# Optimization experiments

Measured on AMD Instinct MI355X. Metric: run time of the kernel, lower is better.

The kernel has to match this reference:

```python
import jax, jax.numpy as jnp
import numpy as np

N = 100_000        # nodes
E = 1_600_000      # edges
IN_F = 128         # input_features
HID = 64           # hiddens per head
OUT = 64           # outputs
NHEADS = 8
ALPHA = 0.2        # leaky_relu negative slope


def setup_inputs() -> dict:
    key = jax.random.key(0)
    ks = jax.random.split(key, 8)
    x = jax.random.normal(ks[0], (N, IN_F), jnp.float32)
    edges = jax.random.randint(ks[1], (2, E), 0, N)
    # nn.Linear(input_features, input_features)
    W0 = jax.random.normal(ks[2], (IN_F, IN_F), jnp.float32) / np.sqrt(IN_F).astype(np.float32)
    b0 = jnp.zeros((IN_F,), jnp.float32)
    # per-head SpGAT params: W [in, out], a [2*out]
    W_heads = jax.random.normal(ks[3], (NHEADS, IN_F, HID), jnp.float32) * 0.05
    a_heads = jax.random.normal(ks[4], (NHEADS, 2 * HID), jnp.float32) * 0.05
    W_end = jax.random.normal(ks[5], (NHEADS * HID, OUT), jnp.float32) * 0.05
    a_end = jax.random.normal(ks[6], (2 * OUT,), jnp.float32) * 0.05
    return dict(x=x, edges=edges, W0=W0, b0=b0,
                W_heads=W_heads, a_heads=a_heads, W_end=W_end, a_end=a_end)


def _sp_gat_layer(x, src, dst, W, a, apply_elu):
    """Standard sparse GAT layer (pyGAT SpGraphAttentionLayer).

    score_e = a . [h_src || h_dst];  e = exp(-leaky_relu(score))
    out_i = (sum_{e: src=i} e * h_dst) / (sum_{e: src=i} e)
    """
    n = x.shape[0]
    h = x @ W                      # [N, F]
    F = h.shape[1]
    # a.[h_i||h_j] decomposed into per-node scores to avoid [E, 2F] gather
    s_src = h @ a[:F]              # [N]
    s_dst = h @ a[F:]              # [N]
    score = s_src[src] + s_dst[dst]            # [E]
    edge_e = jnp.exp(-jax.nn.leaky_relu(score, ALPHA))
    rowsum = jax.ops.segment_sum(edge_e, src, num_segments=n)            # [N]
    agg = jax.ops.segment_sum(edge_e[:, None] * h[dst], src, num_segments=n)  # [N, F]
    out = agg / (rowsum[:, None] + 1e-16)
    return jax.nn.elu(out) if apply_elu else out


def reference(x, edges, W0, b0, W_heads, a_heads, W_end, a_end):
    src, dst = edges[0], edges[1]
    xp = x @ W0 + b0                                           # self.layer
    # multi-head attention, concat on feature dim (loop over fixed small head count)
    heads = [_sp_gat_layer(xp, src, dst, W_heads[i], a_heads[i], apply_elu=True)
             for i in range(NHEADS)]
    h = jnp.concatenate(heads, axis=1)                         # [N, NHEADS*HID]
    out = _sp_gat_layer(h, src, dst, W_end, a_end, apply_elu=False)  # [N, OUT]
    return jax.nn.softmax(out, axis=1)
```

## Files before the change

kernel.cpp:

```cpp
#include <hip/hip_runtime.h>


using bf16x8 = __bf16 __attribute__((ext_vector_type(8)));
using f32x4  = float  __attribute__((ext_vector_type(4)));

__device__ __forceinline__ unsigned short f2bf(float f) {
    __bf16 h = (__bf16)f;
    return __builtin_bit_cast(unsigned short, h);
}
__device__ __forceinline__ float bflo(unsigned int u) {
    return __builtin_bit_cast(float, u << 16);
}
__device__ __forceinline__ float bfhi(unsigned int u) {
    return __builtin_bit_cast(float, u & 0xffff0000u);
}
__device__ __forceinline__ float bfs(unsigned short u) {
    return __builtin_bit_cast(float, (unsigned)u << 16);
}
__device__ __forceinline__ int rdlane_i(int v, int l) {
    return __builtin_amdgcn_readlane(v, l);
}
__device__ __forceinline__ float rdlane_f(float v, int l) {
    return __builtin_bit_cast(float, __builtin_amdgcn_readlane(__builtin_bit_cast(int, v), l));
}
__device__ __forceinline__ float exp2fast(float x) {
#if __has_builtin(__builtin_amdgcn_exp2f)
    return __builtin_amdgcn_exp2f(x);
#else
    return exp2f(x);
#endif
}

#define ALPHA_NEG 0.2f
#define LOG2E 1.44269504088896340736f
#define CHUNK 20000

__global__ void pack_all(const float* __restrict__ W0, const float* __restrict__ Wh,
                         const float* __restrict__ We, const float* __restrict__ ah,
                         unsigned short* __restrict__ W0t, unsigned short* __restrict__ Ballt,
                         unsigned short* __restrict__ Wendt, unsigned short* __restrict__ Bscore) {
    int b = blockIdx.x, t = threadIdx.x;
    if (b < 64) {
        int idx = b * 256 + t;
        int n = idx >> 7, k = idx & 127;
        W0t[n * 128 + k] = f2bf(W0[k * 128 + n]);
    } else if (b < 320) {
        int idx = (b - 64) * 256 + t;
        int c = idx >> 7, k = idx & 127;
        int h = c >> 6, f = c & 63;
        Ballt[idx] = f2bf(Wh[(h * 128 + k) * 64 + f]);
    } else if (b < 448) {
        int idx = (b - 320) * 256 + t;
        int n = idx >> 9, k = idx & 511;
        Wendt[idx] = f2bf(We[k * 64 + n]);
    } else {
        int idx = (b - 448) * 256 + t;
        if (idx < 1024) {
            int h = idx >> 7, k = idx & 127;
            float s = 0.f, d = 0.f;
            for (int f = 0; f < 64; f++) {
                float wv = Wh[(h * 128 + k) * 64 + f];
                s += wv * ah[h * 128 + f];
                d += wv * ah[h * 128 + 64 + f];
            }
            Bscore[h * 128 + k] = f2bf(s * LOG2E);
            Bscore[(8 + h) * 128 + k] = f2bf(d * LOG2E);
        }
    }
}

__global__ void edge_rank(const int* __restrict__ src, int* __restrict__ deg,
                          int* __restrict__ rank, int E) {
    int i = blockIdx.x * 256 + threadIdx.x;
    if (i >= E) return;
    rank[i] = atomicAdd(&deg[src[i]], 1);
}
__global__ void edge_place(const int* __restrict__ src, const int* __restrict__ dst,
                           const int* __restrict__ row_ptr, const int* __restrict__ rank,
                           int* __restrict__ dstp, int E) {
    int i = blockIdx.x * 256 + threadIdx.x;
    if (i >= E) return;
    dstp[row_ptr[src[i]] + rank[i]] = dst[i];
}

#define SCAN_BS 256
__global__ void scan_blocks(const int* __restrict__ deg, int* __restrict__ incl,
                            int* __restrict__ partials, int n) {
    __shared__ int s[SCAN_BS];
    int t = threadIdx.x, i = blockIdx.x * SCAN_BS + t;
    int v = (i < n) ? deg[i] : 0;
    s[t] = v; __syncthreads();
    for (int off = 1; off < SCAN_BS; off <<= 1) {
        int add = (t >= off) ? s[t - off] : 0;
        __syncthreads();
        s[t] += add;
        __syncthreads();
    }
    if (i < n) incl[i] = s[t];
    if (t == SCAN_BS - 1) partials[blockIdx.x] = s[t];
}
__global__ void scan_partials(int* __restrict__ partials, int nb) {
    __shared__ int s[512];
    int t = threadIdx.x;
    int v = (t < nb) ? partials[t] : 0;
    s[t] = v; __syncthreads();
    for (int off = 1; off < 512; off <<= 1) {
        int add = (t >= off) ? s[t - off] : 0;
        __syncthreads();
        s[t] += add;
        __syncthreads();
    }
    if (t < nb) partials[t] = s[t] - v;
}
__global__ void finalize_rowptr(const int* __restrict__ deg, const int* __restrict__ incl,
                                const int* __restrict__ partials, int* __restrict__ row_ptr,
                                int n, int E) {
    int i = blockIdx.x * 256 + threadIdx.x;
    if (i < n) {
        row_ptr[i] = incl[i] - deg[i] + partials[i / SCAN_BS];
    } else if (i == n) {
        row_ptr[n] = E;
    }
}

template <int BM, int BN, int K, int WM, int WN, int MT, int NT,
          bool AF32, bool BIAS, bool OBF16, bool ELU, bool BATCHZ>
__launch_bounds__(256)
__global__ void gemm_mfma(const void* __restrict__ Ap, const unsigned short* __restrict__ Bt,
                          const float* __restrict__ bias, void* __restrict__ Cp, int M,
                          int lda, int ldc) {
    constexpr int LDK = 40;
    __shared__ unsigned short As[BM * LDK];
    __shared__ unsigned short Bs[BN * LDK];
    const int t = threadIdx.x;
    const long m0 = (long)blockIdx.x * BM;
    const long n0 = (long)blockIdx.y * BN;
    const int abase = BATCHZ ? blockIdx.z * K : 0;
    const unsigned short* Btz = BATCHZ ? Bt + (size_t)blockIdx.z * BN * K : Bt;
    const long cbase = BATCHZ ? (long)blockIdx.z * BN : 0;
    const int wave = t >> 6, lane = t & 63;
    const int wm = wave / WN, wn = wave % WN;
    const int lrow = lane & 15, lq = lane >> 4;

    f32x4 acc[MT][NT];
#pragma unroll
    for (int a = 0; a < MT; a++)
#pragma unroll
        for (int b = 0; b < NT; b++) acc[a][b] = (f32x4)0.0f;

    for (int kt = 0; kt < K / 32; kt++) {
        const int k0 = kt * 32;
        if constexpr (AF32) {
            const float* A = (const float*)Ap;
#pragma unroll
            for (int it = 0; it < BM * 8 / 256; it++) {
                int L = t + 256 * it;
                int row = L >> 3, kc = (L & 7) * 4;
                long gr = m0 + row;
                float4 v = make_float4(0.f, 0.f, 0.f, 0.f);
                if (gr < M) v = *(const float4*)&A[gr * lda + abase + k0 + kc];
                unsigned int lo = (unsigned)f2bf(v.x) | ((unsigned)f2bf(v.y) << 16);
                unsigned int hi = (unsigned)f2bf(v.z) | ((unsigned)f2bf(v.w) << 16);
                *(uint2*)&As[row * LDK + kc] = make_uint2(lo, hi);
            }
        } else {
            const unsigned short* A = (const unsigned short*)Ap;
#pragma unroll
            for (int it = 0; it < BM * 4 / 256; it++) {
                int L = t + 256 * it;
                int row = L >> 2, kc = (L & 3) * 8;
                long gr = m0 + row;
                uint4 v = make_uint4(0u, 0u, 0u, 0u);
                if (gr < M) v = *(const uint4*)&A[gr * lda + abase + k0 + kc];
                *(uint4*)&As[row * LDK + kc] = v;
            }
        }
#pragma unroll
        for (int it = 0; it < (BN * 4 + 255) / 256; it++) {
            int L = t + 256 * it;
            if (L < BN * 4) {
                int row = L >> 2, kc = (L & 3) * 8;
                *(uint4*)&Bs[row * LDK + kc] = *(const uint4*)&Btz[(n0 + row) * K + k0 + kc];
            }
        }
        __syncthreads();

        bf16x8 af[MT], bfr[NT];
#pragma unroll
        for (int mt = 0; mt < MT; mt++)
            af[mt] = *(const bf16x8*)&As[((wm * MT + mt) * 16 + lrow) * LDK + lq * 8];
#pragma unroll
        for (int nt = 0; nt < NT; nt++)
            bfr[nt] = *(const bf16x8*)&Bs[((wn * NT + nt) * 16 + lrow) * LDK + lq * 8];
#pragma unroll
        for (int mt = 0; mt < MT; mt++)
#pragma unroll
            for (int nt = 0; nt < NT; nt++)
                acc[mt][nt] = __builtin_amdgcn_mfma_f32_16x16x32_bf16(af[mt], bfr[nt],
                                                                     acc[mt][nt], 0, 0, 0);
        __syncthreads();
    }

#pragma unroll
    for (int mt = 0; mt < MT; mt++) {
        long rbase = m0 + (wm * MT + mt) * 16 + lq * 4;
#pragma unroll
        for (int nt = 0; nt < NT; nt++) {
            long col = cbase + n0 + (wn * NT + nt) * 16 + lrow;
            float bv = 0.f;
            if constexpr (BIAS) bv = bias[col];
#pragma unroll
            for (int r = 0; r < 4; r++) {
                long row = rbase + r;
                if (row < M) {
                    float v = acc[mt][nt][r] + bv;
                    if constexpr (ELU) v = v > 0.f ? v : __expf(v) - 1.0f;
                    if constexpr (OBF16)
                        ((unsigned short*)Cp)[row * ldc + col] = f2bf(v);
                    else
                        ((float*)Cp)[row * ldc + col] = v;
                }
            }
        }
    }
}

__global__ void agg_xp(const int* __restrict__ row_ptr, const int* __restrict__ dstp,
                       const float* __restrict__ s16,
                       const unsigned short* __restrict__ xp, unsigned short* __restrict__ z,
                       int n0, int n1) {
    int t = threadIdx.x, wave = t >> 6, lane = t & 63;
    int i = n0 + blockIdx.x * 4 + wave;
    if (i >= n1) return;
    int e0 = __builtin_amdgcn_readfirstlane(row_ptr[i]);
    int e1 = __builtin_amdgcn_readfirstlane(row_ptr[i + 1]);
    const int hl = lane & 7, sub8 = lane >> 3;
    const int voff = lane << 1;
    float ssv = s16[(size_t)i * 16 + hl];
    float acc[16];
#pragma unroll
    for (int c = 0; c < 16; c++) acc[c] = 0.f;
    float rsl = 0.f;

    for (int p = e0; p < e1; p += 8) {
        int idx = p + sub8;
        int cl = idx < e1 ? idx : e1 - 1;
        int jv = dstp[cl];
        float sc = s16[(size_t)(unsigned)jv * 16 + 8 + hl];
        float s = ssv + sc;
        s = fmaxf(s, ALPHA_NEG * s);
        float wv = (idx < e1) ? exp2fast(-s) : 0.f;
        rsl += wv;
        int nem = e1 - p;
        unsigned xv[8];
#pragma unroll
        for (int u = 0; u < 8; u++) {
            if (u < nem) {
                int ju = rdlane_i(jv, u * 8);
                xv[u] = *(const unsigned*)&xp[(size_t)(unsigned)ju * 128 + voff];
            }
        }
#pragma unroll
        for (int u = 0; u < 8; u++) {
            if (u < nem) {
                float lo = bflo(xv[u]), hi = bfhi(xv[u]);
#pragma unroll
                for (int h = 0; h < 8; h++) {
                    float wh = rdlane_f(wv, u * 8 + h);
                    acc[2 * h]     += wh * lo;
                    acc[2 * h + 1] += wh * hi;
                }
            }
        }
    }

    rsl += __shfl_xor(rsl, 8, 64);
    rsl += __shfl_xor(rsl, 16, 64);
    rsl += __shfl_xor(rsl, 32, 64);
    float inv = 1.0f / (rsl + 1e-16f);
    size_t zb = (size_t)(i - n0) * 1024 + voff;
#pragma unroll
    for (int h = 0; h < 8; h++) {
        float ih = rdlane_f(inv, h);
        unsigned pw = (unsigned)f2bf(acc[2 * h] * ih) |
                      ((unsigned)f2bf(acc[2 * h + 1] * ih) << 16);
        *(unsigned*)&z[zb + h * 128] = pw;
    }
}

__global__ void scores2(const unsigned short* __restrict__ h2b, const float* __restrict__ ae,
                        float* __restrict__ ss2, float* __restrict__ sd2, int n) {
    int t = threadIdx.x, wave = t >> 6, lane = t & 63;
    int i = blockIdx.x * 4 + wave;
    if (i >= n) return;
    float v = bfs(h2b[(size_t)i * 64 + lane]);
    float a = v * ae[lane];
    float b = v * ae[64 + lane];
    for (int d = 32; d > 0; d >>= 1) {
        a += __shfl_xor(a, d, 64);
        b += __shfl_xor(b, d, 64);
    }
    if (lane == 0) { ss2[i] = a * LOG2E; sd2[i] = b * LOG2E; }
}

__global__ void agg_final(const int* __restrict__ row_ptr, const int* __restrict__ dstp,
                          const float* __restrict__ ss2, const float* __restrict__ sd2,
                          const unsigned short* __restrict__ h2b, float* __restrict__ out,
                          int n) {
    int t = threadIdx.x, wave = t >> 6, lane = t & 63;
    int i = blockIdx.x * 4 + wave;
    if (i >= n) return;
    int e0 = __builtin_amdgcn_readfirstlane(row_ptr[i]);
    int e1 = __builtin_amdgcn_readfirstlane(row_ptr[i + 1]);
    float ssrc = ss2[i];
    float acc = 0.f, rsl = 0.f;
    for (int base = e0; base < e1; base += 64) {
        int cnt = e1 - base; if (cnt > 64) cnt = 64;
        int jv = 0; float wv = 0.f;
        if (lane < cnt) {
            jv = dstp[base + lane];
            float sc = ssrc + sd2[jv];
            sc = fmaxf(sc, ALPHA_NEG * sc);
            wv = exp2fast(-sc);
        }
        rsl += wv;
        int q = 0;
        for (; q + 8 <= cnt; q += 8) {
            float vv[8], ww[8];
#pragma unroll
            for (int u = 0; u < 8; u++) {
                int j = rdlane_i(jv, q + u);
                vv[u] = bfs(h2b[((size_t)(unsigned)j << 6) + lane]);
                ww[u] = rdlane_f(wv, q + u);
            }
#pragma unroll
            for (int u = 0; u < 8; u++) acc += ww[u] * vv[u];
        }
        for (; q < cnt; q++) {
            int j = rdlane_i(jv, q);
            float w = rdlane_f(wv, q);
            acc += w * bfs(h2b[((size_t)(unsigned)j << 6) + lane]);
        }
    }
    float rs = rsl;
    for (int d = 32; d > 0; d >>= 1) rs += __shfl_xor(rs, d, 64);
    float o = acc / (rs + 1e-16f);
    float m = o;
    for (int d = 32; d > 0; d >>= 1) m = fmaxf(m, __shfl_xor(m, d, 64));
    float e = __expf(o - m);
    float s = e;
    for (int d = 32; d > 0; d >>= 1) s += __shfl_xor(s, d, 64);
    out[(size_t)i * 64 + lane] = e / s;
}

extern "C" void kernel_launch(void* const* d_in, const int* in_sizes, int n_in,
                              void* d_out, int out_size, void* d_ws, size_t ws_size,
                              hipStream_t stream) {
    const float* x  = (const float*)d_in[0];
    const int* edges = (const int*)d_in[1];
    const float* W0 = (const float*)d_in[2];
    const float* b0 = (const float*)d_in[3];
    const float* Wh = (const float*)d_in[4];
    const float* ah = (const float*)d_in[5];
    const float* We = (const float*)d_in[6];
    const float* ae = (const float*)d_in[7];
    float* dout = (float*)d_out;

    const int Nn = in_sizes[0] / 128;
    const int E  = in_sizes[1] / 2;
    const int* src = edges;
    const int* dst = edges + E;

    char* p = (char*)d_ws;
    auto alloc = [&](size_t bytes) -> char* {
        char* r = p;
        p += (bytes + 255) & ~(size_t)255;
        return r;
    };
    unsigned short* W0t   = (unsigned short*)alloc(128 * 128 * 2);
    unsigned short* Ballt = (unsigned short*)alloc(512 * 128 * 2);
    unsigned short* Wendt = (unsigned short*)alloc((size_t)64 * 512 * 2);
    unsigned short* Bscore = (unsigned short*)alloc(16 * 128 * 2);
    int* deg     = (int*)alloc((size_t)Nn * 4);
    int* incl    = (int*)alloc((size_t)Nn * 4);
    int* part    = (int*)alloc(512 * 4);
    int* row_ptr = (int*)alloc((size_t)(Nn + 1) * 4);
    int* dstp    = (int*)alloc((size_t)E * 4);
    float* s16   = (float*)alloc((size_t)Nn * 16 * 4);
    float* ss2   = (float*)alloc((size_t)Nn * 4);
    float* sd2   = (float*)alloc((size_t)Nn * 4);
    unsigned short* xp = (unsigned short*)alloc((size_t)Nn * 128 * 2);
    unsigned short* z  = (unsigned short*)alloc((size_t)CHUNK * 1024 * 2);
    unsigned short* hcat = (unsigned short*)alloc((size_t)Nn * 512 * 2);
    unsigned short* h2b = (unsigned short*)z;
    int* rank = (int*)hcat;

    size_t needed = (size_t)(p - (char*)d_ws);
    if (needed > ws_size) return;

    const int gm = (Nn + 127) / 128;
    const int nScanB = (Nn + SCAN_BS - 1) / SCAN_BS;
    const int eb = (E + 255) / 256;

    hipMemsetAsync(deg, 0, (size_t)Nn * 4, stream);
    pack_all<<<452, 256, 0, stream>>>(W0, Wh, We, ah, W0t, Ballt, Wendt, Bscore);

    edge_rank<<<eb, 256, 0, stream>>>(src, deg, rank, E);
    scan_blocks<<<nScanB, 256, 0, stream>>>(deg, incl, part, Nn);
    scan_partials<<<1, 512, 0, stream>>>(part, nScanB);
    finalize_rowptr<<<(Nn + 256) / 256, 256, 0, stream>>>(deg, incl, part, row_ptr, Nn, E);
    edge_place<<<eb, 256, 0, stream>>>(src, dst, row_ptr, rank, dstp, E);

    gemm_mfma<128, 128, 128, 2, 2, 4, 4, true, true, true, false, false>
        <<<dim3(gm, 1), 256, 0, stream>>>(x, W0t, b0, xp, Nn, 128, 128);

    gemm_mfma<128, 16, 128, 4, 1, 2, 1, false, false, false, false, false>
        <<<dim3(gm, 1), 256, 0, stream>>>(xp, Bscore, nullptr, s16, Nn, 128, 16);

    for (int c0 = 0; c0 < Nn; c0 += CHUNK) {
        int c1 = min(c0 + CHUNK, Nn);
        int Mc = c1 - c0;
        agg_xp<<<(Mc + 3) / 4, 256, 0, stream>>>(row_ptr, dstp, s16, xp, z, c0, c1);
        gemm_mfma<128, 64, 128, 4, 1, 2, 4, false, false, true, true, true>
            <<<dim3((Mc + 127) / 128, 1, 8), 256, 0, stream>>>(
                z, Ballt, nullptr, hcat + (size_t)c0 * 512, Mc, 1024, 512);
    }

    gemm_mfma<128, 64, 512, 4, 1, 2, 4, false, false, true, false, false>
        <<<dim3(gm, 1), 256, 0, stream>>>(hcat, Wendt, nullptr, h2b, Nn, 512, 64);

    scores2<<<(Nn + 3) / 4, 256, 0, stream>>>(h2b, ae, ss2, sd2, Nn);
    agg_final<<<(Nn + 3) / 4, 256, 0, stream>>>(row_ptr, dstp, ss2, sd2, h2b, dout, Nn);
}
```

Before: 587.2 us.

## Fuse CSR edge build into GEMM launches and split degree counters 16 ways

The edge-rank and edge-place passes are merged into the xp GEMM and the score GEMM launches as extra leading blocks, which removes two kernel launches and lets the edge work run alongside the GEMM tiles. Each node's degree counter is split into 16 sub-slots chosen by edge index to reduce atomic contention. The scan and finalize kernels now sum the sub-slots and write per-slot offsets. This costs 16x larger degree and offset arrays plus a bigger memset, and edge order within a row changes, which affects only floating-point summation order.

Measured after the change: 589.4 us. No clear change (+0.4%).

```diff
diff --git a/kernel.cpp b/kernel.cpp
--- a/kernel.cpp
+++ b/kernel.cpp
@@ -69,75 +69,22 @@
     }
 }
 
-__global__ void edge_rank(const int* __restrict__ src, int* __restrict__ deg,
-                          int* __restrict__ rank, int E) {
-    int i = blockIdx.x * 256 + threadIdx.x;
-    if (i >= E) return;
-    rank[i] = atomicAdd(&deg[src[i]], 1);
-}
-__global__ void edge_place(const int* __restrict__ src, const int* __restrict__ dst,
-                           const int* __restrict__ row_ptr, const int* __restrict__ rank,
-                           int* __restrict__ dstp, int E) {
-    int i = blockIdx.x * 256 + threadIdx.x;
-    if (i >= E) return;
-    dstp[row_ptr[src[i]] + rank[i]] = dst[i];
-}
-
-#define SCAN_BS 256
-__global__ void scan_blocks(const int* __restrict__ deg, int* __restrict__ incl,
-                            int* __restrict__ partials, int n) {
-    __shared__ int s[SCAN_BS];
-    int t = threadIdx.x, i = blockIdx.x * SCAN_BS + t;
-    int v = (i < n) ? deg[i] : 0;
-    s[t] = v; __syncthreads();
-    for (int off = 1; off < SCAN_BS; off <<= 1) {
-        int add = (t >= off) ? s[t - off] : 0;
-        __syncthreads();
-        s[t] += add;
-        __syncthreads();
-    }
-    if (i < n) incl[i] = s[t];
-    if (t == SCAN_BS - 1) partials[blockIdx.x] = s[t];
-}
-__global__ void scan_partials(int* __restrict__ partials, int nb) {
-    __shared__ int s[512];
-    int t = threadIdx.x;
-    int v = (t < nb) ? partials[t] : 0;
-    s[t] = v; __syncthreads();
-    for (int off = 1; off < 512; off <<= 1) {
-        int add = (t >= off) ? s[t - off] : 0;
-        __syncthreads();
-        s[t] += add;
-        __syncthreads();
-    }
-    if (t < nb) partials[t] = s[t] - v;
-}
-__global__ void finalize_rowptr(const int* __restrict__ deg, const int* __restrict__ incl,
-                                const int* __restrict__ partials, int* __restrict__ row_ptr,
-                                int n, int E) {
-    int i = blockIdx.x * 256 + threadIdx.x;
-    if (i < n) {
-        row_ptr[i] = incl[i] - deg[i] + partials[i / SCAN_BS];
-    } else if (i == n) {
-        row_ptr[n] = E;
-    }
-}
-
 template <int BM, int BN, int K, int WM, int WN, int MT, int NT,
           bool AF32, bool BIAS, bool OBF16, bool ELU, bool BATCHZ>
-__launch_bounds__(256)
-__global__ void gemm_mfma(const void* __restrict__ Ap, const unsigned short* __restrict__ Bt,
-                          const float* __restrict__ bias, void* __restrict__ Cp, int M,
-                          int lda, int ldc) {
+__device__ __forceinline__ void gemm_core(const void* __restrict__ Ap,
+                                          const unsigned short* __restrict__ Bt,
+                                          const float* __restrict__ bias,
+                                          void* __restrict__ Cp, int M,
+                                          int lda, int ldc, int bx, int bz) {
     constexpr int LDK = 40;
     __shared__ unsigned short As[BM * LDK];
     __shared__ unsigned short Bs[BN * LDK];
     const int t = threadIdx.x;
-    const long m0 = (long)blockIdx.x * BM;
-    const long n0 = (long)blockIdx.y * BN;
-    const int abase = BATCHZ ? blockIdx.z * K : 0;
-    const unsigned short* Btz = BATCHZ ? Bt + (size_t)blockIdx.z * BN * K : Bt;
-    const long cbase = BATCHZ ? (long)blockIdx.z * BN : 0;
+    const long m0 = (long)bx * BM;
+    const long n0 = 0;
+    const int abase = BATCHZ ? bz * K : 0;
+    const unsigned short* Btz = BATCHZ ? Bt + (size_t)bz * BN * K : Bt;
+    const long cbase = BATCHZ ? (long)bz * BN : 0;
     const int wave = t >> 6, lane = t & 63;
     const int wm = wave / WN, wn = wave % WN;
     const int lrow = lane & 15, lq = lane >> 4;
@@ -222,6 +169,105 @@
                 }
             }
         }
+    }
+}
+
+template <int BM, int BN, int K, int WM, int WN, int MT, int NT,
+          bool AF32, bool BIAS, bool OBF16, bool ELU, bool BATCHZ>
+__launch_bounds__(256)
+__global__ void gemm_mfma(const void* __restrict__ Ap, const unsigned short* __restrict__ Bt,
+                          const float* __restrict__ bias, void* __restrict__ Cp, int M,
+                          int lda, int ldc) {
+    gemm_core<BM, BN, K, WM, WN, MT, NT, AF32, BIAS, OBF16, ELU, BATCHZ>(
+        Ap, Bt, bias, Cp, M, lda, ldc, blockIdx.x, blockIdx.z);
+}
+
+template <int BM, int BN, int K, int WM, int WN, int MT, int NT,
+          bool AF32, bool BIAS, bool OBF16, bool ELU, int MODE>
+__launch_bounds__(256)
+__global__ void fused_gemm_edge(const void* __restrict__ Ap,
+                                const unsigned short* __restrict__ Bt,
+                                const float* __restrict__ bias, void* __restrict__ Cp,
+                                int M, int lda, int ldc,
+                                const int* __restrict__ src, const int* __restrict__ dst,
+                                int* __restrict__ tab,
+                                int* __restrict__ rank, int* __restrict__ dstp,
+                                int E, int eb) {
+    if ((int)blockIdx.x < eb) {
+        int i = blockIdx.x * 256 + threadIdx.x;
+        if (i < E) {
+            int s = src[i];
+            int slot = (s << 4) + (i & 15);
+            if constexpr (MODE == 0) {
+                rank[i] = atomicAdd(&tab[slot], 1);
+            } else {
+                dstp[tab[slot] + rank[i]] = dst[i];
+            }
+        }
+        return;
+    }
+    gemm_core<BM, BN, K, WM, WN, MT, NT, AF32, BIAS, OBF16, ELU, false>(
+        Ap, Bt, bias, Cp, M, lda, ldc, blockIdx.x - eb, 0);
+}
+
+#define SCAN_BS 256
+__global__ void scan_blocks(const int* __restrict__ deg16, int* __restrict__ incl,
+                            int* __restrict__ partials, int n) {
+    __shared__ int s[SCAN_BS];
+    int t = threadIdx.x, i = blockIdx.x * SCAN_BS + t;
+    int v = 0;
+    if (i < n) {
+        const int4* q = (const int4*)&deg16[(size_t)i * 16];
+        int4 a = q[0], b = q[1], c = q[2], d = q[3];
+        v = a.x + a.y + a.z + a.w + b.x + b.y + b.z + b.w +
+            c.x + c.y + c.z + c.w + d.x + d.y + d.z + d.w;
+    }
+    s[t] = v; __syncthreads();
+    for (int off = 1; off < SCAN_BS; off <<= 1) {
+        int add = (t >= off) ? s[t - off] : 0;
+        __syncthreads();
+        s[t] += add;
+        __syncthreads();
+    }
+    if (i < n) incl[i] = s[t];
+    if (t == SCAN_BS - 1) partials[blockIdx.x] = s[t];
+}
+__global__ void scan_partials(int* __restrict__ partials, int nb) {
+    __shared__ int s[512];
+    int t = threadIdx.x;
+    int v = (t < nb) ? partials[t] : 0;
+    s[t] = v; __syncthreads();
+    for (int off = 1; off < 512; off <<= 1) {
+        int add = (t >= off) ? s[t - off] : 0;
+        __syncthreads();
+        s[t] += add;
+        __syncthreads();
+    }
+    if (t < nb) partials[t] = s[t] - v;
+}
+__global__ void finalize_rowptr(const int* __restrict__ deg16, const int* __restrict__ incl,
+                                const int* __restrict__ partials, int* __restrict__ row_ptr,
+                                int* __restrict__ off16, int n, int E) {
+    int i = blockIdx.x * 256 + threadIdx.x;
+    if (i < n) {
+        const int4* q = (const int4*)&deg16[(size_t)i * 16];
+        int dg[16];
+        *(int4*)&dg[0]  = q[0]; *(int4*)&dg[4]  = q[1];
+        *(int4*)&dg[8]  = q[2]; *(int4*)&dg[12] = q[3];
+        int tot = 0;
+#pragma unroll
+        for (int s = 0; s < 16; s++) tot += dg[s];
+        int base = incl[i] - tot + partials[i / SCAN_BS];
+        row_ptr[i] = base;
+        int o[16];
+        int run = base;
+#pragma unroll
+        for (int s = 0; s < 16; s++) { o[s] = run; run += dg[s]; }
+        int4* w = (int4*)&off16[(size_t)i * 16];
+        w[0] = *(int4*)&o[0];  w[1] = *(int4*)&o[4];
+        w[2] = *(int4*)&o[8];  w[3] = *(int4*)&o[12];
+    } else if (i == n) {
+        row_ptr[n] = E;
     }
 }
 
@@ -381,7 +427,8 @@
     unsigned short* Ballt = (unsigned short*)alloc(512 * 128 * 2);
     unsigned short* Wendt = (unsigned short*)alloc((size_t)64 * 512 * 2);
     unsigned short* Bscore = (unsigned short*)alloc(16 * 128 * 2);
-    int* deg     = (int*)alloc((size_t)Nn * 4);
+    int* deg16   = (int*)alloc((size_t)Nn * 16 * 4);
+    int* off16   = (int*)alloc((size_t)Nn * 16 * 4);
     int* incl    = (int*)alloc((size_t)Nn * 4);
     int* part    = (int*)alloc(512 * 4);
     int* row_ptr = (int*)alloc((size_t)(Nn + 1) * 4);
@@ -402,20 +449,21 @@
     const int nScanB = (Nn + SCAN_BS - 1) / SCAN_BS;
     const int eb = (E + 255) / 256;
 
-    hipMemsetAsync(deg, 0, (size_t)Nn * 4, stream);
+    hipMemsetAsync(deg16, 0, (size_t)Nn * 16 * 4, stream);
     pack_all<<<452, 256, 0, stream>>>(W0, Wh, We, ah, W0t, Ballt, Wendt, Bscore);
 
-    edge_rank<<<eb, 256, 0, stream>>>(src, deg, rank, E);
-    scan_blocks<<<nScanB, 256, 0, stream>>>(deg, incl, part, Nn);
+    fused_gemm_edge<128, 128, 128, 2, 2, 4, 4, true, true, true, false, 0>
+        <<<eb + gm, 256, 0, stream>>>(x, W0t, b0, xp, Nn, 128, 128,
+                                      src, dst, deg16, rank, dstp, E, eb);
+
+    scan_blocks<<<nScanB, 256, 0, stream>>>(deg16, incl, part, Nn);
     scan_partials<<<1, 512, 0, stream>>>(part, nScanB);
-    finalize_rowptr<<<(Nn + 256) / 256, 256, 0, stream>>>(deg, incl, part, row_ptr, Nn, E);
-    edge_place<<<eb, 256, 0, stream>>>(src, dst, row_ptr, rank, dstp, E);
-
-    gemm_mfma<128, 128, 128, 2, 2, 4, 4, true, true, true, false, false>
-        <<<dim3(gm, 1), 256, 0, stream>>>(x, W0t, b0, xp, Nn, 128, 128);
-
-    gemm_mfma<128, 16, 128, 4, 1, 2, 1, false, false, false, false, false>
-        <<<dim3(gm, 1), 256, 0, stream>>>(xp, Bscore, nullptr, s16, Nn, 128, 16);
+    finalize_rowptr<<<(Nn + 256) / 256, 256, 0, stream>>>(deg16, incl, part, row_ptr,
+                                                          off16, Nn, E);
+
+    fused_gemm_edge<128, 16, 128, 4, 1, 2, 1, false, false, false, false, 1>
+        <<<eb + gm, 256, 0, stream>>>(xp, Bscore, nullptr, s16, Nn, 128, 16,
+                                      src, dst, off16, rank, dstp, E, eb);
 
     for (int c0 = 0; c0 < Nn; c0 += CHUNK) {
         int c1 = min(c0 + CHUNK, Nn);
```

## Build CSR with two-level bucket sort using shared-memory atomics

Applied to the files above, without the earlier changes.

Replaces the per-edge global atomicAdd degree count, multi-kernel scan and scatter with a two-level bucket sort. Edges are first binned by src>>8 using per-block LDS histograms and a single scan kernel, then scattered as (src,dst) pairs. A per-bucket kernel computes row_ptr and places dst within each bucket using LDS atomics. This removes the memset and the high-contention global atomics over 100k counters. In exchange it adds an extra pass over 8-byte pairs and a serial single-block scan over the block histograms.

Result: faster. 560.3 us (-4.6%).

```diff
diff --git a/kernel.cpp b/kernel.cpp
--- a/kernel.cpp
+++ b/kernel.cpp
@@ -34,6 +34,8 @@
 #define ALPHA_NEG 0.2f
 #define LOG2E 1.44269504088896340736f
 #define CHUNK 20000
+#define TILE 4096
+#define VPT 16
 
 __global__ void pack_all(const float* __restrict__ W0, const float* __restrict__ Wh,
                          const float* __restrict__ We, const float* __restrict__ ah,
@@ -69,57 +71,99 @@
     }
 }
 
-__global__ void edge_rank(const int* __restrict__ src, int* __restrict__ deg,
-                          int* __restrict__ rank, int E) {
-    int i = blockIdx.x * 256 + threadIdx.x;
-    if (i >= E) return;
-    rank[i] = atomicAdd(&deg[src[i]], 1);
-}
-__global__ void edge_place(const int* __restrict__ src, const int* __restrict__ dst,
-                           const int* __restrict__ row_ptr, const int* __restrict__ rank,
-                           int* __restrict__ dstp, int E) {
-    int i = blockIdx.x * 256 + threadIdx.x;
-    if (i >= E) return;
-    dstp[row_ptr[src[i]] + rank[i]] = dst[i];
-}
-
-#define SCAN_BS 256
-__global__ void scan_blocks(const int* __restrict__ deg, int* __restrict__ incl,
-                            int* __restrict__ partials, int n) {
-    __shared__ int s[SCAN_BS];
-    int t = threadIdx.x, i = blockIdx.x * SCAN_BS + t;
-    int v = (i < n) ? deg[i] : 0;
-    s[t] = v; __syncthreads();
-    for (int off = 1; off < SCAN_BS; off <<= 1) {
-        int add = (t >= off) ? s[t - off] : 0;
-        __syncthreads();
-        s[t] += add;
-        __syncthreads();
-    }
-    if (i < n) incl[i] = s[t];
-    if (t == SCAN_BS - 1) partials[blockIdx.x] = s[t];
-}
-__global__ void scan_partials(int* __restrict__ partials, int nb) {
+__global__ void csr_hist(const int* __restrict__ src, int* __restrict__ hb, int E) {
+    __shared__ int h[512];
+    int t = threadIdx.x, blk = blockIdx.x;
+    h[t] = 0; h[t + 256] = 0;
+    __syncthreads();
+    int base = blk * TILE + t;
+#pragma unroll
+    for (int v = 0; v < VPT; v++) {
+        int e = base + v * 256;
+        if (e < E) atomicAdd(&h[src[e] >> 8], 1);
+    }
+    __syncthreads();
+    hb[blk * 512 + t] = h[t];
+    hb[blk * 512 + t + 256] = h[t + 256];
+}
+
+__global__ void csr_scan(int* __restrict__ hb, int* __restrict__ bkt_base, int ablk) {
     __shared__ int s[512];
     int t = threadIdx.x;
-    int v = (t < nb) ? partials[t] : 0;
-    s[t] = v; __syncthreads();
+    int run = 0;
+    for (int b0 = 0; b0 < ablk; b0 += 8) {
+        int vv[8];
+#pragma unroll
+        for (int u = 0; u < 8; u++) {
+            int blk = b0 + u;
+            vv[u] = (blk < ablk) ? hb[blk * 512 + t] : 0;
+        }
+#pragma unroll
+        for (int u = 0; u < 8; u++) {
+            int blk = b0 + u;
+            if (blk < ablk) hb[blk * 512 + t] = run;
+            run += vv[u];
+        }
+    }
+    s[t] = run;
+    __syncthreads();
     for (int off = 1; off < 512; off <<= 1) {
         int add = (t >= off) ? s[t - off] : 0;
         __syncthreads();
         s[t] += add;
         __syncthreads();
     }
-    if (t < nb) partials[t] = s[t] - v;
-}
-__global__ void finalize_rowptr(const int* __restrict__ deg, const int* __restrict__ incl,
-                                const int* __restrict__ partials, int* __restrict__ row_ptr,
-                                int n, int E) {
-    int i = blockIdx.x * 256 + threadIdx.x;
-    if (i < n) {
-        row_ptr[i] = incl[i] - deg[i] + partials[i / SCAN_BS];
-    } else if (i == n) {
-        row_ptr[n] = E;
+    bkt_base[t] = s[t] - run;
+}
+
+__global__ void csr_scatter(const int* __restrict__ src, const int* __restrict__ dst,
+                            const int* __restrict__ hb, const int* __restrict__ bkt_base,
+                            int2* __restrict__ pairs, int E) {
+    __shared__ int cur[512];
+    int t = threadIdx.x, blk = blockIdx.x;
+    cur[t]       = hb[blk * 512 + t]       + bkt_base[t];
+    cur[t + 256] = hb[blk * 512 + t + 256] + bkt_base[t + 256];
+    __syncthreads();
+    int base = blk * TILE + t;
+#pragma unroll
+    for (int v = 0; v < VPT; v++) {
+        int e = base + v * 256;
+        if (e < E) {
+            int sv = src[e], dv = dst[e];
+            int pos = atomicAdd(&cur[sv >> 8], 1);
+            pairs[pos] = make_int2(sv, dv);
+        }
+    }
+}
+
+__global__ void csr_build(const int2* __restrict__ pairs, const int* __restrict__ bkt_base,
+                          int* __restrict__ row_ptr, int* __restrict__ dstp, int n) {
+    __shared__ int h[256];
+    __shared__ int sc[256];
+    int t = threadIdx.x, b = blockIdx.x;
+    int e0 = bkt_base[b], e1 = bkt_base[b + 1];
+    h[t] = 0;
+    __syncthreads();
+    for (int e = e0 + t; e < e1; e += 256) atomicAdd(&h[pairs[e].x & 255], 1);
+    __syncthreads();
+    int v = h[t];
+    sc[t] = v;
+    __syncthreads();
+    for (int off = 1; off < 256; off <<= 1) {
+        int add = (t >= off) ? sc[t - off] : 0;
+        __syncthreads();
+        sc[t] += add;
+        __syncthreads();
+    }
+    int excl = sc[t] - v;
+    int gid = (b << 8) + t;
+    if (gid <= n) row_ptr[gid] = e0 + excl;
+    h[t] = excl;
+    __syncthreads();
+    for (int e = e0 + t; e < e1; e += 256) {
+        int2 pr = pairs[e];
+        int pos = atomicAdd(&h[pr.x & 255], 1);
+        dstp[e0 + pos] = pr.y;
     }
 }
 
@@ -381,9 +425,9 @@
     unsigned short* Ballt = (unsigned short*)alloc(512 * 128 * 2);
     unsigned short* Wendt = (unsigned short*)alloc((size_t)64 * 512 * 2);
     unsigned short* Bscore = (unsigned short*)alloc(16 * 128 * 2);
-    int* deg     = (int*)alloc((size_t)Nn * 4);
-    int* incl    = (int*)alloc((size_t)Nn * 4);
-    int* part    = (int*)alloc(512 * 4);
+    const int ablk = (E + TILE - 1) / TILE;
+    int* hist_blk = (int*)alloc((size_t)ablk * 512 * 4);
+    int* bkt_base = (int*)alloc(512 * 4);
     int* row_ptr = (int*)alloc((size_t)(Nn + 1) * 4);
     int* dstp    = (int*)alloc((size_t)E * 4);
     float* s16   = (float*)alloc((size_t)Nn * 16 * 4);
@@ -393,23 +437,20 @@
     unsigned short* z  = (unsigned short*)alloc((size_t)CHUNK * 1024 * 2);
     unsigned short* hcat = (unsigned short*)alloc((size_t)Nn * 512 * 2);
     unsigned short* h2b = (unsigned short*)z;
-    int* rank = (int*)hcat;
+    int2* pairs = (int2*)hcat;
 
     size_t needed = (size_t)(p - (char*)d_ws);
     if (needed > ws_size) return;
 
     const int gm = (Nn + 127) / 128;
-    const int nScanB = (Nn + SCAN_BS - 1) / SCAN_BS;
-    const int eb = (E + 255) / 256;
-
-    hipMemsetAsync(deg, 0, (size_t)Nn * 4, stream);
+    const int nbkt = (Nn + 255) >> 8;
+
     pack_all<<<452, 256, 0, stream>>>(W0, Wh, We, ah, W0t, Ballt, Wendt, Bscore);
 
-    edge_rank<<<eb, 256, 0, stream>>>(src, deg, rank, E);
-    scan_blocks<<<nScanB, 256, 0, stream>>>(deg, incl, part, Nn);
-    scan_partials<<<1, 512, 0, stream>>>(part, nScanB);
-    finalize_rowptr<<<(Nn + 256) / 256, 256, 0, stream>>>(deg, incl, part, row_ptr, Nn, E);
-    edge_place<<<eb, 256, 0, stream>>>(src, dst, row_ptr, rank, dstp, E);
+    csr_hist<<<ablk, 256, 0, stream>>>(src, hist_blk, E);
+    csr_scan<<<1, 512, 0, stream>>>(hist_blk, bkt_base, ablk);
+    csr_scatter<<<ablk, 256, 0, stream>>>(src, dst, hist_blk, bkt_base, pairs, E);
+    csr_build<<<nbkt, 256, 0, stream>>>(pairs, bkt_base, row_ptr, dstp, Nn);
 
     gemm_mfma<128, 128, 128, 2, 2, 4, 4, true, true, true, false, false>
         <<<dim3(gm, 1), 256, 0, stream>>>(x, W0t, b0, xp, Nn, 128, 128);
```
